# Optimization experiments

Hardware: AMD Instinct MI355X
Metric: run time of the kernel (lower is better)

## Reference

```python
import jax, jax.numpy as jnp
import numpy as np

EPS = 1e-12  # F.normalize eps

def setup_inputs() -> dict:
    key = jax.random.key(0)
    k1, k2 = jax.random.split(key)
    B, T, D = 4, 4096, 1024
    x = jax.random.normal(k1, (B, T, D), dtype=jnp.float32)
    V = jax.random.normal(k2, (T, T), dtype=jnp.float32) * 0.02
    bias = jnp.zeros((1, 1, D // 2), dtype=jnp.float32)
    return {"x": x, "V": V, "bias": bias}

def reference(x, V, bias):
    # x: [B, T, mt_dim]; V: [T, T]; bias: [1, 1, mt_half]
    mt_half = x.shape[-1] // 2
    x_left = x[..., :mt_half]
    x_right = x[..., mt_half:]
    # L2 normalize along last dim (torch F.normalize semantics)
    norm = jnp.sqrt(jnp.sum(x_right * x_right, axis=-1, keepdims=True))
    xn = x_right / jnp.maximum(norm, EPS)
    # cosine similarity [B, T, T]
    sim = jnp.einsum('bqd,bkd->bqk', xn, xn)
    weighted = V[None, :, :] * sim
    # chunked path of the original applies second bmm to the NORMALIZED right half
    ctx = jnp.einsum('bqk,bkd->bqd', weighted, xn)
    gate = jax.nn.sigmoid(ctx + bias)
    return x_left * gate
```

## Files before the change

### kernel.cpp

```cpp
#include <hip/hip_runtime.h>
#include <stdint.h>

typedef _Float16 half8 __attribute__((ext_vector_type(8)));
typedef _Float16 half4v __attribute__((ext_vector_type(4)));
typedef float floatx4 __attribute__((ext_vector_type(4)));
typedef float floatx16 __attribute__((ext_vector_type(16)));
typedef long long i64v;

#define TT 4096
#define DH 512

#define WAITLGKM() asm volatile("s_waitcnt lgkmcnt(0)" ::: "memory")
#define BAR() __builtin_amdgcn_s_barrier()
#define FENCE() asm volatile("" ::: "memory")

__device__ __forceinline__ unsigned short f2h(float f) {
    union { _Float16 h; unsigned short u; } v;
    v.h = (_Float16)f;
    return v.u;
}

__global__ void norm_k(const float* __restrict__ x, unsigned short* __restrict__ xn,
                       unsigned char* __restrict__ xn8) {
    const int w = threadIdx.x >> 6, l = threadIdx.x & 63;
    const int row = blockIdx.x * 4 + w;
    const float* src = x + (size_t)row * 1024 + 512 + l * 8;
    floatx4 a = *(const floatx4*)src;
    floatx4 c = *(const floatx4*)(src + 4);
    float s = a[0]*a[0] + a[1]*a[1] + a[2]*a[2] + a[3]*a[3]
            + c[0]*c[0] + c[1]*c[1] + c[2]*c[2] + c[3]*c[3];
    #pragma unroll
    for (int off = 32; off > 0; off >>= 1) s += __shfl_xor(s, off);
    const float scale = 1.0f / fmaxf(sqrtf(s), 1e-12f);
    float v[8] = {a[0], a[1], a[2], a[3], c[0], c[1], c[2], c[3]};
    uint32_t pk[4];
    #pragma unroll
    for (int i = 0; i < 4; i++)
        pk[i] = (uint32_t)f2h(v[2*i] * scale) | ((uint32_t)f2h(v[2*i+1] * scale) << 16);
    uint4 o; o.x = pk[0]; o.y = pk[1]; o.z = pk[2]; o.w = pk[3];
    *(uint4*)(xn + (size_t)row * DH + l * 8) = o;
    const float s16 = scale * 16.0f;
    int pa = __builtin_amdgcn_cvt_pk_fp8_f32(v[0]*s16, v[1]*s16, 0, 0);
    pa     = __builtin_amdgcn_cvt_pk_fp8_f32(v[2]*s16, v[3]*s16, pa, 1);
    int pb = __builtin_amdgcn_cvt_pk_fp8_f32(v[4]*s16, v[5]*s16, 0, 0);
    pb     = __builtin_amdgcn_cvt_pk_fp8_f32(v[6]*s16, v[7]*s16, pb, 1);
    uint2 o8; o8.x = (uint32_t)pa; o8.y = (uint32_t)pb;
    *(uint2*)(xn8 + (size_t)row * DH + l * 8) = o8;
}

__global__ void transpose_k(const unsigned short* __restrict__ xn,
                            unsigned char* __restrict__ xnT8) {
    __shared__ __align__(16) unsigned short tile[64 * 72];
    const int b = blockIdx.z;
    const int t0 = blockIdx.x * 64, d0 = blockIdx.y * 64;
    const int tid = threadIdx.x;
    #pragma unroll
    for (int i = 0; i < 2; i++) {
        int c = i * 256 + tid;
        int tr = c >> 3, d8 = c & 7;
        uint4 vv = *(const uint4*)(xn + ((size_t)(b * TT + t0 + tr) * DH + d0 + d8 * 8));
        *(uint4*)&tile[tr * 72 + d8 * 8] = vv;
    }
    __syncthreads();
    #pragma unroll
    for (int i = 0; i < 2; i++) {
        int c = i * 256 + tid;
        int dd = c >> 3, t8 = c & 7;
        float f[8];
        #pragma unroll
        for (int k = 0; k < 8; k++) {
            unsigned short u = tile[(t8 * 8 + k) * 72 + dd];
            f[k] = (float)(*(const _Float16*)&u) * 16.0f;
        }
        int pa = __builtin_amdgcn_cvt_pk_fp8_f32(f[0], f[1], 0, 0);
        pa     = __builtin_amdgcn_cvt_pk_fp8_f32(f[2], f[3], pa, 1);
        int pb = __builtin_amdgcn_cvt_pk_fp8_f32(f[4], f[5], 0, 0);
        pb     = __builtin_amdgcn_cvt_pk_fp8_f32(f[6], f[7], pb, 1);
        uint2 o8; o8.x = (uint32_t)pa; o8.y = (uint32_t)pb;
        *(uint2*)(xnT8 + ((size_t)(b * DH + d0 + dd) * TT + t0 + t8 * 8)) = o8;
    }
}

__global__ __launch_bounds__(512, 2) void fused_k(
    const unsigned char* __restrict__ xn8, const unsigned char* __restrict__ xnT8,
    const float* __restrict__ V, const float* __restrict__ bias,
    const float* __restrict__ x, float* __restrict__ out)
{
    __shared__ __align__(16) unsigned char smemB[98304];
    unsigned char*  kn8B  = smemB;
    unsigned char*  kt8B  = smemB + 32768;
    unsigned short* SredL = (unsigned short*)(smemB + 65536);

    const int tid = threadIdx.x;
    const int w = tid >> 6, l = tid & 63;
    const int h = l >> 5, m32 = l & 31;
    const int g = w >> 2, mi = (w >> 1) & 1, dh = w & 1;
    const int p = g * 2 + dh;
    const int wk0 = g * 256 + dh * 128;
    const int wd0 = w * 64;

    const int flat = blockIdx.y * 64 + blockIdx.x;
    const int work = (flat & 7) * 32 + (flat >> 3);
    const int b = work >> 6, qt = work & 63;
    const int q0 = qt * 64;

    const unsigned char* x8b = xn8  + (size_t)b * TT * DH;
    const unsigned char* xt8 = xnT8 + (size_t)b * DH * TT;

    unsigned char* knP8 = kn8B + w * 4096;
    unsigned char* ktP8 = kt8B + w * 4096;

    const int tq = tid >> 3, to = tid & 7;
    const float* vptr = V + (size_t)(q0 + tq) * TT + to * 8;
    const int keyR = tq & 15;
    const int aLo = ((to * 2    ) ^ keyR) * 4;
    const int aHi = ((to * 2 + 1) ^ keyR) * 4;

    i64v qf8[2][8];
    #pragma unroll
    for (int ni = 0; ni < 2; ni++)
        #pragma unroll
        for (int ks = 0; ks < 8; ks++)
            qf8[ni][ks] = *(const i64v*)(x8b + (size_t)(q0 + ni*32 + m32) * DH
                                         + wk0 + ks*16 + h*8);
    FENCE();
    #pragma unroll
    for (int i = 0; i < 4; i++) {
        int r = i * 8 + (l >> 3);
        int dg = (l & 7) ^ (r & 7);
        const unsigned char* gp = x8b + (size_t)(mi*32 + r) * DH + wk0 + dg * 16;
        __builtin_amdgcn_global_load_lds(
            (const __attribute__((address_space(1))) void*)gp,
            (__attribute__((address_space(3))) void*)&knP8[i * 1024], 16, 0, 0);
    }
    FENCE();
    #pragma unroll
    for (int i = 0; i < 4; i++) {
        int dr = i * 16 + (l >> 2);
        int cs = (l & 3) ^ ((dr >> 1) & 3);
        const unsigned char* gp = xt8 + (size_t)(wd0 + dr) * TT + cs * 16;
        __builtin_amdgcn_global_load_lds(
            (const __attribute__((address_space(1))) void*)gp,
            (__attribute__((address_space(3))) void*)&ktP8[i * 1024], 16, 0, 0);
    }
    FENCE();
    floatx4 vf0 = *(const floatx4*)(vptr);
    floatx4 vf1 = *(const floatx4*)(vptr + 4);

    floatx16 acc[2][2];
    #pragma unroll
    for (int i = 0; i < 2; i++)
        #pragma unroll
        for (int j = 0; j < 2; j++)
            acc[i][j] = (floatx16)(0.f);

    #pragma unroll 1
    for (int t = 0; t < 64; t++) {
        asm volatile("s_waitcnt vmcnt(6)" ::: "memory");

        floatx16 s0 = (floatx16)(0.f), s1 = (floatx16)(0.f);
        __builtin_amdgcn_s_setprio(1);
        #pragma unroll
        for (int ks = 0; ks < 8; ks++) {
            i64v a8 = *(const i64v*)&knP8[m32 * 128 + ((ks ^ (m32 & 7)) * 16) + h * 8];
            s0 = __builtin_amdgcn_mfma_f32_32x32x16_fp8_fp8(a8, qf8[0][ks], s0, 0, 0, 0);
            s1 = __builtin_amdgcn_mfma_f32_32x32x16_fp8_fp8(a8, qf8[1][ks], s1, 0, 0, 0);
        }
        __builtin_amdgcn_s_setprio(0);

        #pragma unroll
        for (int ni = 0; ni < 2; ni++) {
            const int q = ni * 32 + m32;
            unsigned short* sp = SredL + p * 4096 + q * 64;
            const int key = q & 15;
            #pragma unroll
            for (int rr = 0; rr < 4; rr++) {
                int u = (mi * 8 + rr * 2 + h) ^ key;
                half4v v4;
                if (ni == 0) {
                    v4[0]=(_Float16)s0[rr*4+0]; v4[1]=(_Float16)s0[rr*4+1];
                    v4[2]=(_Float16)s0[rr*4+2]; v4[3]=(_Float16)s0[rr*4+3];
                } else {
                    v4[0]=(_Float16)s1[rr*4+0]; v4[1]=(_Float16)s1[rr*4+1];
                    v4[2]=(_Float16)s1[rr*4+2]; v4[3]=(_Float16)s1[rr*4+3];
                }
                *(half4v*)&sp[u * 4] = v4;
            }
        }
        if (t < 63) {
            FENCE();
            #pragma unroll
            for (int i = 0; i < 4; i++) {
                int r = i * 8 + (l >> 3);
                int dg = (l & 7) ^ (r & 7);
                const unsigned char* gp = x8b + (size_t)((t+1)*64 + mi*32 + r) * DH + wk0 + dg * 16;
                __builtin_amdgcn_global_load_lds(
                    (const __attribute__((address_space(1))) void*)gp,
                    (__attribute__((address_space(3))) void*)&knP8[i * 1024], 16, 0, 0);
            }
            FENCE();
        }
        WAITLGKM();
        BAR();

        half4v l0 = *(const half4v*)&SredL[        tq * 64 + aLo];
        half4v h0 = *(const half4v*)&SredL[        tq * 64 + aHi];
        half4v l1 = *(const half4v*)&SredL[4096  + tq * 64 + aLo];
        half4v h1 = *(const half4v*)&SredL[4096  + tq * 64 + aHi];
        half4v l2 = *(const half4v*)&SredL[8192  + tq * 64 + aLo];
        half4v h2 = *(const half4v*)&SredL[8192  + tq * 64 + aHi];
        half4v l3 = *(const half4v*)&SredL[12288 + tq * 64 + aLo];
        half4v h3 = *(const half4v*)&SredL[12288 + tq * 64 + aHi];
        half4v sLo = (l0 + l1) + (l2 + l3);
        half4v sHi = (h0 + h1) + (h2 + h3);
        if (t < 63) { asm volatile("s_waitcnt vmcnt(4)" ::: "memory"); }
        else        { asm volatile("s_waitcnt vmcnt(0)" ::: "memory"); }
        {
            float w0 = (float)sLo[0]*vf0[0], w1 = (float)sLo[1]*vf0[1];
            float w2 = (float)sLo[2]*vf0[2], w3 = (float)sLo[3]*vf0[3];
            float w4 = (float)sHi[0]*vf1[0], w5 = (float)sHi[1]*vf1[1];
            float w6 = (float)sHi[2]*vf1[2], w7 = (float)sHi[3]*vf1[3];
            int pa = __builtin_amdgcn_cvt_pk_fp8_f32(w0, w1, 0, 0);
            pa     = __builtin_amdgcn_cvt_pk_fp8_f32(w2, w3, pa, 1);
            int pb = __builtin_amdgcn_cvt_pk_fp8_f32(w4, w5, 0, 0);
            pb     = __builtin_amdgcn_cvt_pk_fp8_f32(w6, w7, pb, 1);
            uint2 w8w; w8w.x = (uint32_t)pa; w8w.y = (uint32_t)pb;
            *(uint2*)((unsigned char*)SredL + tq * 128 + ((2*to) ^ keyR) * 8) = w8w;
        }
        WAITLGKM();
        BAR();

        const unsigned char* W8 = (const unsigned char*)SredL;
        const int keyA = m32 & 15;
        const int k2 = (m32 >> 1) & 3;
        __builtin_amdgcn_s_setprio(1);
        #pragma unroll
        for (int ks = 0; ks < 4; ks++) {
            const int u0 = ks * 4 + h * 2;
            i64v wf0 = *(const i64v*)&W8[(m32     ) * 128 + ((u0 ^ keyA) * 8)];
            i64v wf1 = *(const i64v*)&W8[(32 + m32) * 128 + ((u0 ^ keyA) * 8)];
            const int ko = ((ks ^ k2) * 16) + h * 8;
            i64v kf0 = *(const i64v*)&ktP8[(m32     ) * 64 + ko];
            i64v kf1 = *(const i64v*)&ktP8[(32 + m32) * 64 + ko];
            acc[0][0] = __builtin_amdgcn_mfma_f32_32x32x16_fp8_fp8(wf0, kf0, acc[0][0], 0, 0, 0);
            acc[0][1] = __builtin_amdgcn_mfma_f32_32x32x16_fp8_fp8(wf0, kf1, acc[0][1], 0, 0, 0);
            acc[1][0] = __builtin_amdgcn_mfma_f32_32x32x16_fp8_fp8(wf1, kf0, acc[1][0], 0, 0, 0);
            acc[1][1] = __builtin_amdgcn_mfma_f32_32x32x16_fp8_fp8(wf1, kf1, acc[1][1], 0, 0, 0);
        }
        __builtin_amdgcn_s_setprio(0);
        if (t < 63) {
            FENCE();
            #pragma unroll
            for (int i = 0; i < 4; i++) {
                int dr = i * 16 + (l >> 2);
                int cs = (l & 3) ^ ((dr >> 1) & 3);
                const unsigned char* gp = xt8 + (size_t)(wd0 + dr) * TT + (t+1)*64 + cs * 16;
                __builtin_amdgcn_global_load_lds(
                    (const __attribute__((address_space(1))) void*)gp,
                    (__attribute__((address_space(3))) void*)&ktP8[i * 1024], 16, 0, 0);
            }
            FENCE();
            vf0 = *(const floatx4*)(vptr + (t+1)*64);
            vf1 = *(const floatx4*)(vptr + (t+1)*64 + 4);
            FENCE();
        }
        WAITLGKM();
        BAR();
    }

    const float* xb = x + (size_t)b * TT * 1024;
    float* ob = out + (size_t)b * TT * DH;
    const float isc = 1.0f / 4096.0f;
    #pragma unroll
    for (int mi2 = 0; mi2 < 2; mi2++)
        #pragma unroll
        for (int nd = 0; nd < 2; nd++) {
            int d = wd0 + nd * 32 + m32;
            float bv = bias[d];
            #pragma unroll
            for (int r = 0; r < 16; r++) {
                int q = q0 + mi2 * 32 + (r & 3) + 8 * (r >> 2) + 4 * h;
                float cv = acc[mi2][nd][r] * isc + bv;
                float gate = 1.0f / (1.0f + __expf(-cv));
                ob[(size_t)q * DH + d] = xb[(size_t)q * 1024 + d] * gate;
            }
        }
}

extern "C" void kernel_launch(void* const* d_in, const int* in_sizes, int n_in,
                              void* d_out, int out_size, void* d_ws, size_t ws_size,
                              hipStream_t stream) {
    const float* x    = (const float*)d_in[0];
    const float* V    = (const float*)d_in[1];
    const float* bias = (const float*)d_in[2];
    float* out = (float*)d_out;

    unsigned short* xn   = (unsigned short*)d_ws;
    unsigned char*  xn8  = (unsigned char*)(xn + (size_t)4 * TT * DH);
    unsigned char*  xnT8 = xn8 + (size_t)4 * TT * DH;

    norm_k<<<dim3(4 * TT / 4), 256, 0, stream>>>(x, xn, xn8);
    transpose_k<<<dim3(TT / 64, DH / 64, 4), 256, 0, stream>>>(xn, xnT8);
    fused_k<<<dim3(TT / 64, 4), 512, 0, stream>>>(xn8, xnT8, V, bias, x, out);
}
```

Baseline: 159.2 us.

## Warp-specialize fused kernel into producer S-waves and consumer PV-waves

Splits the 8 waves into 4 producer waves that compute the full-K similarity tile (no cross-wave half-precision reduction through LDS) and 4 consumer waves that run the second GEMM one tile behind. K tiles and the weighted tile are double-buffered in LDS, which removes one barrier phase per iteration and lets the two GEMMs overlap. Producers hold 32 Q fragments in registers, and LDS grows to 104KB. With launch_bounds(512,2), two blocks would need about 208KB of LDS, so occupancy may drop.

```diff
diff --git a/kernel.cpp b/kernel.cpp
--- a/kernel.cpp
+++ b/kernel.cpp
@@ -2,7 +2,6 @@
 #include <stdint.h>
 
 typedef _Float16 half8 __attribute__((ext_vector_type(8)));
-typedef _Float16 half4v __attribute__((ext_vector_type(4)));
 typedef float floatx4 __attribute__((ext_vector_type(4)));
 typedef float floatx16 __attribute__((ext_vector_type(16)));
 typedef long long i64v;
@@ -86,18 +85,14 @@
     const float* __restrict__ V, const float* __restrict__ bias,
     const float* __restrict__ x, float* __restrict__ out)
 {
-    __shared__ __align__(16) unsigned char smemB[98304];
-    unsigned char*  kn8B  = smemB;
-    unsigned char*  kt8B  = smemB + 32768;
-    unsigned short* SredL = (unsigned short*)(smemB + 65536);
+    __shared__ __align__(16) unsigned char smemB[106496];
+    unsigned char* kn8B = smemB;
+    unsigned char* kt8B = smemB + 65536;
+    unsigned char* W8B  = smemB + 98304;
 
     const int tid = threadIdx.x;
     const int w = tid >> 6, l = tid & 63;
     const int h = l >> 5, m32 = l & 31;
-    const int g = w >> 2, mi = (w >> 1) & 1, dh = w & 1;
-    const int p = g * 2 + dh;
-    const int wk0 = g * 256 + dh * 128;
-    const int wd0 = w * 64;
 
     const int flat = blockIdx.y * 64 + blockIdx.x;
     const int work = (flat & 7) * 32 + (flat >> 3);
@@ -107,184 +102,203 @@
     const unsigned char* x8b = xn8  + (size_t)b * TT * DH;
     const unsigned char* xt8 = xnT8 + (size_t)b * DH * TT;
 
-    unsigned char* knP8 = kn8B + w * 4096;
-    unsigned char* ktP8 = kt8B + w * 4096;
-
-    const int tq = tid >> 3, to = tid & 7;
-    const float* vptr = V + (size_t)(q0 + tq) * TT + to * 8;
-    const int keyR = tq & 15;
-    const int aLo = ((to * 2    ) ^ keyR) * 4;
-    const int aHi = ((to * 2 + 1) ^ keyR) * 4;
-
-    i64v qf8[2][8];
-    #pragma unroll
-    for (int ni = 0; ni < 2; ni++)
-        #pragma unroll
-        for (int ks = 0; ks < 8; ks++)
-            qf8[ni][ks] = *(const i64v*)(x8b + (size_t)(q0 + ni*32 + m32) * DH
-                                         + wk0 + ks*16 + h*8);
-    FENCE();
-    #pragma unroll
-    for (int i = 0; i < 4; i++) {
-        int r = i * 8 + (l >> 3);
-        int dg = (l & 7) ^ (r & 7);
-        const unsigned char* gp = x8b + (size_t)(mi*32 + r) * DH + wk0 + dg * 16;
-        __builtin_amdgcn_global_load_lds(
-            (const __attribute__((address_space(1))) void*)gp,
-            (__attribute__((address_space(3))) void*)&knP8[i * 1024], 16, 0, 0);
+    if (w < 4) {
+        const int mi = w & 1, ni = (w >> 1) & 1;
+        const int q = ni * 32 + m32;
+        const float* vrow = V + (size_t)(q0 + q) * TT + mi * 32 + 4 * h;
+        const int wkey = q & 15;
+        const int srow = ni * 16 + ((l >> 5) ? 1 : 0);
+
+        i64v qf8[32];
+        #pragma unroll
+        for (int ks = 0; ks < 32; ks++)
+            qf8[ks] = *(const i64v*)(x8b + (size_t)(q0 + q) * DH + ks * 16 + h * 8);
+        FENCE();
+        #pragma unroll
+        for (int i = 0; i < 8; i++) {
+            int r = ni * 16 + i * 2 + (l >> 5);
+            int u16 = (l & 31) ^ r;
+            const unsigned char* gp = x8b + (size_t)(mi * 32 + r) * DH + u16 * 16;
+            __builtin_amdgcn_global_load_lds(
+                (const __attribute__((address_space(1))) void*)gp,
+                (__attribute__((address_space(3))) void*)&kn8B[mi * 16384 + (ni * 16 + i * 2) * 512], 16, 0, 0);
+        }
+        FENCE();
+        floatx4 vf0 = *(const floatx4*)(vrow);
+        floatx4 vf1 = *(const floatx4*)(vrow + 8);
+        floatx4 vf2 = *(const floatx4*)(vrow + 16);
+        floatx4 vf3 = *(const floatx4*)(vrow + 24);
+        asm volatile("s_waitcnt vmcnt(4)" ::: "memory");
+        BAR();
+
+        #pragma unroll 1
+        for (int t = 0; t < 64; t++) {
+            if (t < 63) {
+                #pragma unroll
+                for (int i = 0; i < 8; i++) {
+                    int r = ni * 16 + i * 2 + (l >> 5);
+                    int u16 = (l & 31) ^ r;
+                    const unsigned char* gp = x8b + (size_t)((t+1)*64 + mi*32 + r) * DH + u16 * 16;
+                    __builtin_amdgcn_global_load_lds(
+                        (const __attribute__((address_space(1))) void*)gp,
+                        (__attribute__((address_space(3))) void*)
+                            &kn8B[((t+1) & 1) * 32768 + mi * 16384 + (ni * 16 + i * 2) * 512], 16, 0, 0);
+                }
+                FENCE();
+            }
+            const unsigned char* arow = kn8B + (t & 1) * 32768 + mi * 16384 + m32 * 512;
+            floatx16 s0 = (floatx16)(0.f), s1 = (floatx16)(0.f);
+            floatx16 s2 = (floatx16)(0.f), s3 = (floatx16)(0.f);
+            __builtin_amdgcn_s_setprio(1);
+            #pragma unroll
+            for (int ks = 0; ks < 8; ks++) {
+                i64v a0 = *(const i64v*)&arow[((ks      ) ^ m32) * 16 + h * 8];
+                i64v a1 = *(const i64v*)&arow[((ks +  8) ^ m32) * 16 + h * 8];
+                i64v a2 = *(const i64v*)&arow[((ks + 16) ^ m32) * 16 + h * 8];
+                i64v a3 = *(const i64v*)&arow[((ks + 24) ^ m32) * 16 + h * 8];
+                s0 = __builtin_amdgcn_mfma_f32_32x32x16_fp8_fp8(a0, qf8[ks     ], s0, 0, 0, 0);
+                s1 = __builtin_amdgcn_mfma_f32_32x32x16_fp8_fp8(a1, qf8[ks +  8], s1, 0, 0, 0);
+                s2 = __builtin_amdgcn_mfma_f32_32x32x16_fp8_fp8(a2, qf8[ks + 16], s2, 0, 0, 0);
+                s3 = __builtin_amdgcn_mfma_f32_32x32x16_fp8_fp8(a3, qf8[ks + 24], s3, 0, 0, 0);
+            }
+            __builtin_amdgcn_s_setprio(0);
+            floatx16 s = (s0 + s1) + (s2 + s3);
+            {
+                unsigned char* Wb = W8B + (t & 1) * 4096 + q * 64;
+                int p0 = __builtin_amdgcn_cvt_pk_fp8_f32(s[0]*vf0[0],  s[1]*vf0[1],  0, 0);
+                p0     = __builtin_amdgcn_cvt_pk_fp8_f32(s[2]*vf0[2],  s[3]*vf0[3],  p0, 1);
+                int p1 = __builtin_amdgcn_cvt_pk_fp8_f32(s[4]*vf1[0],  s[5]*vf1[1],  0, 0);
+                p1     = __builtin_amdgcn_cvt_pk_fp8_f32(s[6]*vf1[2],  s[7]*vf1[3],  p1, 1);
+                int p2 = __builtin_amdgcn_cvt_pk_fp8_f32(s[8]*vf2[0],  s[9]*vf2[1],  0, 0);
+                p2     = __builtin_amdgcn_cvt_pk_fp8_f32(s[10]*vf2[2], s[11]*vf2[3], p2, 1);
+                int p3 = __builtin_amdgcn_cvt_pk_fp8_f32(s[12]*vf3[0], s[13]*vf3[1], 0, 0);
+                p3     = __builtin_amdgcn_cvt_pk_fp8_f32(s[14]*vf3[2], s[15]*vf3[3], p3, 1);
+                *(uint32_t*)&Wb[((mi*8 + 0 + h) ^ wkey) * 4] = (uint32_t)p0;
+                *(uint32_t*)&Wb[((mi*8 + 2 + h) ^ wkey) * 4] = (uint32_t)p1;
+                *(uint32_t*)&Wb[((mi*8 + 4 + h) ^ wkey) * 4] = (uint32_t)p2;
+                *(uint32_t*)&Wb[((mi*8 + 6 + h) ^ wkey) * 4] = (uint32_t)p3;
+            }
+            if (t < 63) {
+                FENCE();
+                vf0 = *(const floatx4*)(vrow + (t+1)*64);
+                vf1 = *(const floatx4*)(vrow + (t+1)*64 + 8);
+                vf2 = *(const floatx4*)(vrow + (t+1)*64 + 16);
+                vf3 = *(const floatx4*)(vrow + (t+1)*64 + 24);
+                FENCE();
+            }
+            WAITLGKM();
+            if (t < 63) { asm volatile("s_waitcnt vmcnt(4)" ::: "memory"); }
+            BAR();
+        }
+    } else {
+        const int cw = w - 4;
+        unsigned char* ktS = kt8B + cw * 8192;
+        const int db = cw * 128;
+        const int keyW = m32 & 15;
+        const int kk2 = (m32 >> 1) & 3;
+
+        floatx16 acc[2][4];
+        #pragma unroll
+        for (int i = 0; i < 2; i++)
+            #pragma unroll
+            for (int j = 0; j < 4; j++)
+                acc[i][j] = (floatx16)(0.f);
+
+        #pragma unroll
+        for (int i = 0; i < 8; i++) {
+            int dr = i * 16 + (l >> 2);
+            int cs = (l & 3) ^ ((dr >> 1) & 3);
+            const unsigned char* gp = xt8 + (size_t)(db + dr) * TT + cs * 16;
+            __builtin_amdgcn_global_load_lds(
+                (const __attribute__((address_space(1))) void*)gp,
+                (__attribute__((address_space(3))) void*)&ktS[i * 1024], 16, 0, 0);
+        }
+        FENCE();
+        BAR();
+
+        #pragma unroll 1
+        for (int t = 0; t < 64; t++) {
+            if (t >= 1) {
+                asm volatile("s_waitcnt vmcnt(0)" ::: "memory");
+                const unsigned char* Wb = W8B + ((t - 1) & 1) * 4096;
+                __builtin_amdgcn_s_setprio(1);
+                #pragma unroll
+                for (int ks = 0; ks < 4; ks++) {
+                    union { uint32_t u[2]; i64v v; } wf0, wf1;
+                    wf0.u[0] = *(const uint32_t*)&Wb[(m32     ) * 64 + ((ks*4 + 2*h    ) ^ keyW) * 4];
+                    wf0.u[1] = *(const uint32_t*)&Wb[(m32     ) * 64 + ((ks*4 + 2*h + 1) ^ keyW) * 4];
+                    wf1.u[0] = *(const uint32_t*)&Wb[(32 + m32) * 64 + ((ks*4 + 2*h    ) ^ keyW) * 4];
+                    wf1.u[1] = *(const uint32_t*)&Wb[(32 + m32) * 64 + ((ks*4 + 2*h + 1) ^ keyW) * 4];
+                    i64v kf[4];
+                    #pragma unroll
+                    for (int nd = 0; nd < 4; nd++) {
+                        int dr = nd * 32 + m32;
+                        kf[nd] = *(const i64v*)&ktS[dr * 64 + ((ks ^ kk2) * 16) + h * 8];
+                    }
+                    #pragma unroll
+                    for (int nd = 0; nd < 4; nd++) {
+                        acc[0][nd] = __builtin_amdgcn_mfma_f32_32x32x16_fp8_fp8(wf0.v, kf[nd], acc[0][nd], 0, 0, 0);
+                        acc[1][nd] = __builtin_amdgcn_mfma_f32_32x32x16_fp8_fp8(wf1.v, kf[nd], acc[1][nd], 0, 0, 0);
+                    }
+                }
+                __builtin_amdgcn_s_setprio(0);
+                WAITLGKM();
+                FENCE();
+                #pragma unroll
+                for (int i = 0; i < 8; i++) {
+                    int dr = i * 16 + (l >> 2);
+                    int cs = (l & 3) ^ ((dr >> 1) & 3);
+                    const unsigned char* gp = xt8 + (size_t)(db + dr) * TT + t * 64 + cs * 16;
+                    __builtin_amdgcn_global_load_lds(
+                        (const __attribute__((address_space(1))) void*)gp,
+                        (__attribute__((address_space(3))) void*)&ktS[i * 1024], 16, 0, 0);
+                }
+                FENCE();
+            }
+            BAR();
+        }
+        {
+            asm volatile("s_waitcnt vmcnt(0)" ::: "memory");
+            const unsigned char* Wb = W8B + (63 & 1) * 4096;
+            #pragma unroll
+            for (int ks = 0; ks < 4; ks++) {
+                union { uint32_t u[2]; i64v v; } wf0, wf1;
+                wf0.u[0] = *(const uint32_t*)&Wb[(m32     ) * 64 + ((ks*4 + 2*h    ) ^ keyW) * 4];
+                wf0.u[1] = *(const uint32_t*)&Wb[(m32     ) * 64 + ((ks*4 + 2*h + 1) ^ keyW) * 4];
+                wf1.u[0] = *(const uint32_t*)&Wb[(32 + m32) * 64 + ((ks*4 + 2*h    ) ^ keyW) * 4];
+                wf1.u[1] = *(const uint32_t*)&Wb[(32 + m32) * 64 + ((ks*4 + 2*h + 1) ^ keyW) * 4];
+                i64v kf[4];
+                #pragma unroll
+                for (int nd = 0; nd < 4; nd++) {
+                    int dr = nd * 32 + m32;
+                    kf[nd] = *(const i64v*)&ktS[dr * 64 + ((ks ^ kk2) * 16) + h * 8];
+                }
+                #pragma unroll
+                for (int nd = 0; nd < 4; nd++) {
+                    acc[0][nd] = __builtin_amdgcn_mfma_f32_32x32x16_fp8_fp8(wf0.v, kf[nd], acc[0][nd], 0, 0, 0);
+                    acc[1][nd] = __builtin_amdgcn_mfma_f32_32x32x16_fp8_fp8(wf1.v, kf[nd], acc[1][nd], 0, 0, 0);
+                }
+            }
+        }
+
+        const float* xb = x + (size_t)b * TT * 1024;
+        float* ob = out + (size_t)b * TT * DH;
+        const float isc = 1.0f / 4096.0f;
+        #pragma unroll
+        for (int ai = 0; ai < 2; ai++)
+            #pragma unroll
+            for (int nd = 0; nd < 4; nd++) {
+                int d = db + nd * 32 + m32;
+                float bv = bias[d];
+                #pragma unroll
+                for (int r = 0; r < 16; r++) {
+                    int q = q0 + ai * 32 + (r & 3) + 8 * (r >> 2) + 4 * h;
+                    float cv = acc[ai][nd][r] * isc + bv;
+                    float gate = 1.0f / (1.0f + __expf(-cv));
+                    ob[(size_t)q * DH + d] = xb[(size_t)q * 1024 + d] * gate;
+                }
+            }
     }
-    FENCE();
-    #pragma unroll
-    for (int i = 0; i < 4; i++) {
-        int dr = i * 16 + (l >> 2);
-        int cs = (l & 3) ^ ((dr >> 1) & 3);
-        const unsigned char* gp = xt8 + (size_t)(wd0 + dr) * TT + cs * 16;
-        __builtin_amdgcn_global_load_lds(
-            (const __attribute__((address_space(1))) void*)gp,
-            (__attribute__((address_space(3))) void*)&ktP8[i * 1024], 16, 0, 0);
-    }
-    FENCE();
-    floatx4 vf0 = *(const floatx4*)(vptr);
-    floatx4 vf1 = *(const floatx4*)(vptr + 4);
-
-    floatx16 acc[2][2];
-    #pragma unroll
-    for (int i = 0; i < 2; i++)
-        #pragma unroll
-        for (int j = 0; j < 2; j++)
-            acc[i][j] = (floatx16)(0.f);
-
-    #pragma unroll 1
-    for (int t = 0; t < 64; t++) {
-        asm volatile("s_waitcnt vmcnt(6)" ::: "memory");
-
-        floatx16 s0 = (floatx16)(0.f), s1 = (floatx16)(0.f);
-        __builtin_amdgcn_s_setprio(1);
-        #pragma unroll
-        for (int ks = 0; ks < 8; ks++) {
-            i64v a8 = *(const i64v*)&knP8[m32 * 128 + ((ks ^ (m32 & 7)) * 16) + h * 8];
-            s0 = __builtin_amdgcn_mfma_f32_32x32x16_fp8_fp8(a8, qf8[0][ks], s0, 0, 0, 0);
-            s1 = __builtin_amdgcn_mfma_f32_32x32x16_fp8_fp8(a8, qf8[1][ks], s1, 0, 0, 0);
-        }
-        __builtin_amdgcn_s_setprio(0);
-
-        #pragma unroll
-        for (int ni = 0; ni < 2; ni++) {
-            const int q = ni * 32 + m32;
-            unsigned short* sp = SredL + p * 4096 + q * 64;
-            const int key = q & 15;
-            #pragma unroll
-            for (int rr = 0; rr < 4; rr++) {
-                int u = (mi * 8 + rr * 2 + h) ^ key;
-                half4v v4;
-                if (ni == 0) {
-                    v4[0]=(_Float16)s0[rr*4+0]; v4[1]=(_Float16)s0[rr*4+1];
-                    v4[2]=(_Float16)s0[rr*4+2]; v4[3]=(_Float16)s0[rr*4+3];
-                } else {
-                    v4[0]=(_Float16)s1[rr*4+0]; v4[1]=(_Float16)s1[rr*4+1];
-                    v4[2]=(_Float16)s1[rr*4+2]; v4[3]=(_Float16)s1[rr*4+3];
-                }
-                *(half4v*)&sp[u * 4] = v4;
-            }
-        }
-        if (t < 63) {
-            FENCE();
-            #pragma unroll
-            for (int i = 0; i < 4; i++) {
-                int r = i * 8 + (l >> 3);
-                int dg = (l & 7) ^ (r & 7);
-                const unsigned char* gp = x8b + (size_t)((t+1)*64 + mi*32 + r) * DH + wk0 + dg * 16;
-                __builtin_amdgcn_global_load_lds(
-                    (const __attribute__((address_space(1))) void*)gp,
-                    (__attribute__((address_space(3))) void*)&knP8[i * 1024], 16, 0, 0);
-            }
-            FENCE();
-        }
-        WAITLGKM();
-        BAR();
-
-        half4v l0 = *(const half4v*)&SredL[        tq * 64 + aLo];
-        half4v h0 = *(const half4v*)&SredL[        tq * 64 + aHi];
-        half4v l1 = *(const half4v*)&SredL[4096  + tq * 64 + aLo];
-        half4v h1 = *(const half4v*)&SredL[4096  + tq * 64 + aHi];
-        half4v l2 = *(const half4v*)&SredL[8192  + tq * 64 + aLo];
-        half4v h2 = *(const half4v*)&SredL[8192  + tq * 64 + aHi];
-        half4v l3 = *(const half4v*)&SredL[12288 + tq * 64 + aLo];
-        half4v h3 = *(const half4v*)&SredL[12288 + tq * 64 + aHi];
-        half4v sLo = (l0 + l1) + (l2 + l3);
-        half4v sHi = (h0 + h1) + (h2 + h3);
-        if (t < 63) { asm volatile("s_waitcnt vmcnt(4)" ::: "memory"); }
-        else        { asm volatile("s_waitcnt vmcnt(0)" ::: "memory"); }
-        {
-            float w0 = (float)sLo[0]*vf0[0], w1 = (float)sLo[1]*vf0[1];
-            float w2 = (float)sLo[2]*vf0[2], w3 = (float)sLo[3]*vf0[3];
-            float w4 = (float)sHi[0]*vf1[0], w5 = (float)sHi[1]*vf1[1];
-            float w6 = (float)sHi[2]*vf1[2], w7 = (float)sHi[3]*vf1[3];
-            int pa = __builtin_amdgcn_cvt_pk_fp8_f32(w0, w1, 0, 0);
-            pa     = __builtin_amdgcn_cvt_pk_fp8_f32(w2, w3, pa, 1);
-            int pb = __builtin_amdgcn_cvt_pk_fp8_f32(w4, w5, 0, 0);
-            pb     = __builtin_amdgcn_cvt_pk_fp8_f32(w6, w7, pb, 1);
-            uint2 w8w; w8w.x = (uint32_t)pa; w8w.y = (uint32_t)pb;
-            *(uint2*)((unsigned char*)SredL + tq * 128 + ((2*to) ^ keyR) * 8) = w8w;
-        }
-        WAITLGKM();
-        BAR();
-
-        const unsigned char* W8 = (const unsigned char*)SredL;
-        const int keyA = m32 & 15;
-        const int k2 = (m32 >> 1) & 3;
-        __builtin_amdgcn_s_setprio(1);
-        #pragma unroll
-        for (int ks = 0; ks < 4; ks++) {
-            const int u0 = ks * 4 + h * 2;
-            i64v wf0 = *(const i64v*)&W8[(m32     ) * 128 + ((u0 ^ keyA) * 8)];
-            i64v wf1 = *(const i64v*)&W8[(32 + m32) * 128 + ((u0 ^ keyA) * 8)];
-            const int ko = ((ks ^ k2) * 16) + h * 8;
-            i64v kf0 = *(const i64v*)&ktP8[(m32     ) * 64 + ko];
-            i64v kf1 = *(const i64v*)&ktP8[(32 + m32) * 64 + ko];
-            acc[0][0] = __builtin_amdgcn_mfma_f32_32x32x16_fp8_fp8(wf0, kf0, acc[0][0], 0, 0, 0);
-            acc[0][1] = __builtin_amdgcn_mfma_f32_32x32x16_fp8_fp8(wf0, kf1, acc[0][1], 0, 0, 0);
-            acc[1][0] = __builtin_amdgcn_mfma_f32_32x32x16_fp8_fp8(wf1, kf0, acc[1][0], 0, 0, 0);
-            acc[1][1] = __builtin_amdgcn_mfma_f32_32x32x16_fp8_fp8(wf1, kf1, acc[1][1], 0, 0, 0);
-        }
-        __builtin_amdgcn_s_setprio(0);
-        if (t < 63) {
-            FENCE();
-            #pragma unroll
-            for (int i = 0; i < 4; i++) {
-                int dr = i * 16 + (l >> 2);
-                int cs = (l & 3) ^ ((dr >> 1) & 3);
-                const unsigned char* gp = xt8 + (size_t)(wd0 + dr) * TT + (t+1)*64 + cs * 16;
-                __builtin_amdgcn_global_load_lds(
-                    (const __attribute__((address_space(1))) void*)gp,
-                    (__attribute__((address_space(3))) void*)&ktP8[i * 1024], 16, 0, 0);
-            }
-            FENCE();
-            vf0 = *(const floatx4*)(vptr + (t+1)*64);
-            vf1 = *(const floatx4*)(vptr + (t+1)*64 + 4);
-            FENCE();
-        }
-        WAITLGKM();
-        BAR();
-    }
-
-    const float* xb = x + (size_t)b * TT * 1024;
-    float* ob = out + (size_t)b * TT * DH;
-    const float isc = 1.0f / 4096.0f;
-    #pragma unroll
-    for (int mi2 = 0; mi2 < 2; mi2++)
-        #pragma unroll
-        for (int nd = 0; nd < 2; nd++) {
-            int d = wd0 + nd * 32 + m32;
-            float bv = bias[d];
-            #pragma unroll
-            for (int r = 0; r < 16; r++) {
-                int q = q0 + mi2 * 32 + (r & 3) + 8 * (r >> 2) + 4 * h;
-                float cv = acc[mi2][nd][r] * isc + bv;
-                float gate = 1.0f / (1.0f + __expf(-cv));
-                ob[(size_t)q * DH + d] = xb[(size_t)q * 1024 + d] * gate;
-            }
-        }
 }
 
 extern "C" void kernel_launch(void* const* d_in, const int* in_sizes, int n_in,
```

Result: faster. 143.7 us (-9.7%).
